# Kernel optimization log

Measured on AMD Instinct MI355X. Metric: run time of the kernel, lower is better.

The kernel has to match this reference:

```python
import math
import jax, jax.numpy as jnp
import numpy as np


def setup_inputs() -> dict:
    key = jax.random.key(0)
    T, C = 8192, 2048
    layer_depth, num_layers = 5, 10
    ks = jax.random.split(key, 8)

    x = jax.random.normal(ks[0], (T, C), jnp.float32)
    sx = jax.random.normal(ks[1], (C,), jnp.float32)
    aa = jnp.zeros((C,), jnp.float32)
    bb = jnp.zeros((C,), jnp.float32)
    pp = jnp.zeros((C,), jnp.float32)

    # parameter initial values per TimeMix.setup
    r01 = layer_depth / (num_layers - 1)
    r10 = 1.0 - layer_depth / num_layers
    zigzag = 0.5 * (jnp.arange(1, C + 1) % 3 - 1).astype(jnp.float32)
    time_first = jnp.full((C,), math.log(0.3), jnp.float32) + zigzag
    h = jnp.arange(C, dtype=jnp.float32)
    time_decay = (-5.0 + 8.0 * (h / (C - 1)) ** (0.7 + 1.3 * r01)).astype(jnp.float32)
    xr = jnp.arange(C, dtype=jnp.float32) / C
    time_mix_k = xr ** r10
    time_mix_v = time_mix_k + 0.3 * r01
    time_mix_r = xr ** (0.5 * r10)

    ln_scale = jnp.ones((C,), jnp.float32)
    ln_bias = jnp.zeros((C,), jnp.float32)

    s = 1.0 / np.sqrt(C)  # lecun-normal-ish scale for Dense kernels
    Wk = jax.random.normal(ks[2], (C, C), jnp.float32) * s
    Wv = jax.random.normal(ks[3], (C, C), jnp.float32) * s
    Wr = jax.random.normal(ks[4], (C, C), jnp.float32) * s
    Wo = jax.random.normal(ks[5], (C, C), jnp.float32) * s

    return dict(x=x, sx=sx, aa=aa, bb=bb, pp=pp,
                time_first=time_first, time_decay=time_decay,
                time_mix_k=time_mix_k, time_mix_v=time_mix_v, time_mix_r=time_mix_r,
                ln_scale=ln_scale, ln_bias=ln_bias,
                Wk=Wk, Wv=Wv, Wr=Wr, Wo=Wo)


def reference(x, sx, aa, bb, pp, time_first, time_decay,
              time_mix_k, time_mix_v, time_mix_r,
              ln_scale, ln_bias, Wk, Wv, Wr, Wo):
    # LayerNorm(eps=1e-5)
    mu = jnp.mean(x, axis=-1, keepdims=True)
    var = jnp.var(x, axis=-1, keepdims=True)
    xx = (x - mu) * jax.lax.rsqrt(var + 1e-5) * ln_scale + ln_bias  # [T, C]

    # token shift: previous timestep (sx state for t=0)
    sxs = jnp.concatenate((sx[None, :], xx[:-1, :]), axis=0)  # [T, C]
    kx = xx * time_mix_k + sxs * (1.0 - time_mix_k)
    vx = xx * time_mix_v + sxs * (1.0 - time_mix_v)
    rx = xx * time_mix_r + sxs * (1.0 - time_mix_r)

    r = jax.nn.sigmoid(rx @ Wr)  # [T, C]
    k = kx @ Wk                  # [T, C]
    v = vx @ Wv                  # [T, C]

    w = -jnp.exp(time_decay)     # [C]

    def step(state, kv):
        aa, bb, pp = state
        kk, vv = kv
        # output with numerically-stable log-sum-exp style bookkeeping
        ww = time_first + kk
        p = jnp.maximum(pp, ww)
        e1 = jnp.exp(pp - p)
        e2 = jnp.exp(ww - p)
        out = ((e1 * aa + e2 * vv) / (e1 * bb + e2)).astype(r.dtype)
        # state update
        ww2 = w + pp
        p2 = jnp.maximum(ww2, kk)
        e1b = jnp.exp(ww2 - p2)
        e2b = jnp.exp(kk - p2)
        aa = e1b * aa + e2b * vv
        bb = e1b * bb + e2b
        return (aa, bb, p2), out

    (aa, bb, pp), wkv = jax.lax.scan(step, (aa, bb, pp), (k, v))  # wkv: [T, C]

    out = x + (r * wkv) @ Wo
    return (out, xx[-1, :], aa, bb, pp)
```

## Files before the change

### kernel.cpp

```cpp
#include <hip/hip_runtime.h>
#include <stdint.h>

#define T_DIM 8192
#define C_DIM 2048
#define LCHUNK 128
#define NCHUNK (T_DIM / LCHUNK)

typedef unsigned short u16;
typedef __bf16 bf16x8_t __attribute__((ext_vector_type(8)));
typedef float f32x4_t __attribute__((ext_vector_type(4)));

__device__ __forceinline__ u16 f2bf(float f) {
    union { float f; uint32_t u; } x; x.f = f;
    uint32_t r = x.u + 0x7fffu + ((x.u >> 16) & 1u);
    return (u16)(r >> 16);
}
__device__ __forceinline__ float bf2f(u16 u) {
    union { uint32_t u; float f; } x; x.u = ((uint32_t)u) << 16;
    return x.f;
}
__device__ __forceinline__ void gload16(const void* g, void* l) {
    __builtin_amdgcn_global_load_lds((const __attribute__((address_space(1))) uint32_t*)g,
                                     (__attribute__((address_space(3))) uint32_t*)l, 16, 0, 0);
}
__device__ __forceinline__ f32x4_t mfma16(bf16x8_t a, bf16x8_t b, f32x4_t c) {
    return __builtin_amdgcn_mfma_f32_16x16x32_bf16(a, b, c, 0, 0, 0);
}

__global__ __launch_bounds__(256)
void transpose_cast(const float* __restrict__ W0, const float* __restrict__ W1,
                    const float* __restrict__ W2, const float* __restrict__ W3,
                    u16* __restrict__ Wt)
{
    __shared__ float tile[32][33];
    const int z = blockIdx.z;
    const float* W = (z == 0) ? W0 : (z == 1) ? W1 : (z == 2) ? W2 : W3;
    u16* Tm = Wt + (size_t)z * C_DIM * C_DIM;
    const int tx = threadIdx.x & 31, ty = threadIdx.x >> 5;
    const int bn = blockIdx.x * 32, bk = blockIdx.y * 32;
#pragma unroll
    for (int i = 0; i < 4; ++i)
        tile[ty + 8 * i][tx] = W[(size_t)(bk + ty + 8 * i) * C_DIM + bn + tx];
    __syncthreads();
#pragma unroll
    for (int i = 0; i < 4; ++i)
        Tm[(size_t)(bn + ty + 8 * i) * C_DIM + bk + tx] = f2bf(tile[tx][ty + 8 * i]);
}

union F8 { float4 v[2]; float f[8]; };

__global__ __launch_bounds__(256)
void ln_mix_kernel(const float* __restrict__ x, const float* __restrict__ sx,
                   const float* __restrict__ lns, const float* __restrict__ lnb,
                   const float* __restrict__ tmk, const float* __restrict__ tmv,
                   const float* __restrict__ tmr,
                   u16* __restrict__ kx, u16* __restrict__ vx, u16* __restrict__ rx,
                   float* __restrict__ xx_last)
{
    const int t = blockIdx.x;
    const int tid = threadIdx.x;
    const size_t rowoff = (size_t)t * C_DIM;

    F8 a, p;
    const float4* xt = (const float4*)(x + rowoff);
    a.v[0] = xt[2 * tid]; a.v[1] = xt[2 * tid + 1];
    const float4* xp = (t == 0) ? (const float4*)sx : (const float4*)(x + rowoff - C_DIM);
    p.v[0] = xp[2 * tid]; p.v[1] = xp[2 * tid + 1];

    float s1 = 0.f, s2 = 0.f, s3 = 0.f, s4 = 0.f;
#pragma unroll
    for (int i = 0; i < 8; ++i) {
        s1 += a.f[i]; s2 += a.f[i] * a.f[i];
        s3 += p.f[i]; s4 += p.f[i] * p.f[i];
    }
#pragma unroll
    for (int off = 32; off; off >>= 1) {
        s1 += __shfl_down(s1, off);
        s2 += __shfl_down(s2, off);
        s3 += __shfl_down(s3, off);
        s4 += __shfl_down(s4, off);
    }
    __shared__ float red[4][4];
    if ((tid & 63) == 0) {
        red[0][tid >> 6] = s1; red[1][tid >> 6] = s2;
        red[2][tid >> 6] = s3; red[3][tid >> 6] = s4;
    }
    __syncthreads();
    s1 = red[0][0] + red[0][1] + red[0][2] + red[0][3];
    s2 = red[1][0] + red[1][1] + red[1][2] + red[1][3];
    s3 = red[2][0] + red[2][1] + red[2][2] + red[2][3];
    s4 = red[3][0] + red[3][1] + red[3][2] + red[3][3];
    const float inv = 1.0f / (float)C_DIM;
    const float mu = s1 * inv;
    const float rstd = rsqrtf(s2 * inv - mu * mu + 1e-5f);
    const float mup = s3 * inv;
    const float rstdp = rsqrtf(s4 * inv - mup * mup + 1e-5f);

    F8 ls, lb, mk, mv, mr;
    { const float4* q = (const float4*)lns; ls.v[0] = q[2*tid]; ls.v[1] = q[2*tid+1]; }
    { const float4* q = (const float4*)lnb; lb.v[0] = q[2*tid]; lb.v[1] = q[2*tid+1]; }
    { const float4* q = (const float4*)tmk; mk.v[0] = q[2*tid]; mk.v[1] = q[2*tid+1]; }
    { const float4* q = (const float4*)tmv; mv.v[0] = q[2*tid]; mv.v[1] = q[2*tid+1]; }
    { const float4* q = (const float4*)tmr; mr.v[0] = q[2*tid]; mr.v[1] = q[2*tid+1]; }

    union { u16 u[8]; uint4 q; } ok, ov, orr;
#pragma unroll
    for (int i = 0; i < 8; ++i) {
        const float xxv  = (a.f[i] - mu) * rstd * ls.f[i] + lb.f[i];
        const float prev = (t == 0) ? p.f[i] : (p.f[i] - mup) * rstdp * ls.f[i] + lb.f[i];
        ok.u[i]  = f2bf(xxv * mk.f[i] + prev * (1.f - mk.f[i]));
        ov.u[i]  = f2bf(xxv * mv.f[i] + prev * (1.f - mv.f[i]));
        orr.u[i] = f2bf(xxv * mr.f[i] + prev * (1.f - mr.f[i]));
        if (t == T_DIM - 1) xx_last[tid * 8 + i] = xxv;
    }
    ((uint4*)(kx + rowoff))[tid] = ok.q;
    ((uint4*)(vx + rowoff))[tid] = ov.q;
    ((uint4*)(rx + rowoff))[tid] = orr.q;
}

__global__ __launch_bounds__(256, 2)
void gemm_tile(const u16* __restrict__ A, const u16* __restrict__ Bt,
               void* __restrict__ Cout, const float* __restrict__ resid,
               const int mode, const int M, const int N, const int K)
{
    __shared__ u16 lds[2 * 12288];
    const int tid = threadIdx.x;
    const int wave = tid >> 6, lane = tid & 63;
    const int nbm = M >> 8;
    const int m0 = (int)(blockIdx.x % nbm) << 8;
    const int n0 = (int)(blockIdx.x / nbm) << 7;
    const int wm = wave >> 1, wn = wave & 1;
    const int fr = lane & 15, fo = lane >> 4;
    const int sw = (fo ^ ((fr >> 1) & 3)) * 8;

    f32x4_t acc[8][4] = {};

    const int lrow = lane >> 2;
    const int scol = ((lane & 3) ^ ((lane >> 3) & 3)) * 8;
    const u16* gA = A  + (size_t)(m0 + wave * 16 + lrow) * K + scol;
    const u16* gB = Bt + (size_t)(n0 + wave * 16 + lrow) * K + scol;
    const int dstw = wave * 512;

    auto stage = [&](int t) {
        const int b = (t & 1) * 12288;
        const u16* ga = gA + (size_t)t * 32;
        const u16* gb = gB + (size_t)t * 32;
        gload16(ga,                   lds + b + dstw);
        gload16(ga + (size_t)64 * K,  lds + b + 2048 + dstw);
        gload16(ga + (size_t)128 * K, lds + b + 4096 + dstw);
        gload16(ga + (size_t)192 * K, lds + b + 6144 + dstw);
        gload16(gb,                   lds + b + 8192 + dstw);
        gload16(gb + (size_t)64 * K,  lds + b + 10240 + dstw);
    };

    const int NT = K >> 5;
    stage(0);
    asm volatile("s_waitcnt vmcnt(0)" ::: "memory");
    asm volatile("s_barrier" ::: "memory");

    for (int t = 0; t < NT; ++t) {
        if (t + 1 < NT) stage(t + 1);
        const u16* lA = lds + (t & 1) * 12288 + (wm * 128 + fr) * 32;
        const u16* lB = lds + (t & 1) * 12288 + 8192 + (wn * 64 + fr) * 32;
        bf16x8_t a[8], b[4];
#pragma unroll
        for (int mi = 0; mi < 8; ++mi) a[mi] = *(const bf16x8_t*)(lA + mi * 512 + sw);
#pragma unroll
        for (int ni = 0; ni < 4; ++ni) b[ni] = *(const bf16x8_t*)(lB + ni * 512 + sw);
        __builtin_amdgcn_s_setprio(1);
#pragma unroll
        for (int mi = 0; mi < 8; ++mi)
#pragma unroll
            for (int ni = 0; ni < 4; ++ni)
                acc[mi][ni] = mfma16(a[mi], b[ni], acc[mi][ni]);
        __builtin_amdgcn_s_setprio(0);
        asm volatile("s_waitcnt vmcnt(0)" ::: "memory");
        asm volatile("s_barrier" ::: "memory");
    }

    const int r4 = fo * 4;
#pragma unroll
    for (int mi = 0; mi < 8; ++mi) {
#pragma unroll
        for (int ni = 0; ni < 4; ++ni) {
            const int col = n0 + wn * 64 + ni * 16 + fr;
#pragma unroll
            for (int i = 0; i < 4; ++i) {
                const int row = m0 + wm * 128 + mi * 16 + r4 + i;
                float v = acc[mi][ni][i];
                if (resid) v += resid[(size_t)row * N + col];
                if (mode == 0)      ((float*)Cout)[(size_t)row * N + col] = v;
                else if (mode == 1) ((u16*)Cout)[(size_t)row * N + col] = f2bf(v);
                else {
                    const float s = 1.f / (1.f + __expf(-v));
                    ((u16*)Cout)[(size_t)row * N + col] = f2bf(s);
                }
            }
        }
    }
}

__global__ __launch_bounds__(256)
void scan_partial(const float* __restrict__ k, const u16* __restrict__ v,
                  const float* __restrict__ time_decay,
                  float* __restrict__ pA, float* __restrict__ pB, float* __restrict__ pP)
{
    const int c = blockIdx.y * 256 + threadIdx.x;
    const int j = blockIdx.x;
    const float w = -__expf(time_decay[c]);
    float aa = 0.f, bb = 0.f, pp = -1e30f;
    const float* kp = k + (size_t)j * LCHUNK * C_DIM + c;
    const u16*  vp = v + (size_t)j * LCHUNK * C_DIM + c;
#pragma unroll 4
    for (int i = 0; i < LCHUNK; ++i) {
        const float kk = *kp;
        const float vv = bf2f(*vp);
        kp += C_DIM; vp += C_DIM;
        const float ww = w + pp;
        const float p2 = fmaxf(ww, kk);
        const float e1 = __expf(ww - p2);
        const float e2 = __expf(kk - p2);
        aa = e1 * aa + e2 * vv;
        bb = e1 * bb + e2;
        pp = p2;
    }
    const int o = j * C_DIM + c;
    pA[o] = aa; pB[o] = bb; pP[o] = pp;
}

__global__ __launch_bounds__(256)
void scan_combine(const float* __restrict__ pA, const float* __restrict__ pB,
                  const float* __restrict__ pP,
                  const float* __restrict__ aa_in, const float* __restrict__ bb_in,
                  const float* __restrict__ pp_in,
                  const float* __restrict__ time_decay,
                  float* __restrict__ sA, float* __restrict__ sB, float* __restrict__ sP)
{
    const int c = blockIdx.x * 256 + threadIdx.x;
    const float wL = -__expf(time_decay[c]) * (float)LCHUNK;
    float a = aa_in[c], b = bb_in[c], p = pp_in[c];
    for (int j = 0; j < NCHUNK; ++j) {
        const int o = j * C_DIM + c;
        sA[o] = a; sB[o] = b; sP[o] = p;
        const float A = pA[o], B = pB[o], P = pP[o];
        const float pd = p + wL;
        const float q = fmaxf(pd, P);
        const float e1 = __expf(pd - q), e2 = __expf(P - q);
        a = e1 * a + e2 * A;
        b = e1 * b + e2 * B;
        p = q;
    }
}

__global__ __launch_bounds__(256)
void scan_out(const float* __restrict__ k, const u16* __restrict__ v,
              const u16* __restrict__ r,
              const float* __restrict__ time_decay, const float* __restrict__ time_first,
              const float* __restrict__ sA, const float* __restrict__ sB,
              const float* __restrict__ sP,
              u16* __restrict__ arwkv,
              float* __restrict__ aa_out, float* __restrict__ bb_out, float* __restrict__ pp_out)
{
    const int c = blockIdx.y * 256 + threadIdx.x;
    const int j = blockIdx.x;
    const float w = -__expf(time_decay[c]);
    const float u = time_first[c];
    const int so = j * C_DIM + c;
    float aa = sA[so], bb = sB[so], pp = sP[so];
    const size_t base = (size_t)j * LCHUNK * C_DIM + c;
    const float* kp = k + base;
    const u16*  vp = v + base;
    const u16*  rp = r + base;
    u16* op = arwkv + base;
#pragma unroll 4
    for (int i = 0; i < LCHUNK; ++i) {
        const float kk = *kp;
        const float vv = bf2f(*vp);
        const float sr = bf2f(*rp);
        kp += C_DIM; vp += C_DIM; rp += C_DIM;
        const float ww = u + kk;
        const float p = fmaxf(pp, ww);
        const float e1 = __expf(pp - p);
        const float e2 = __expf(ww - p);
        const float out = (e1 * aa + e2 * vv) / (e1 * bb + e2);
        *op = f2bf(sr * out);
        op += C_DIM;
        const float ww2 = w + pp;
        const float p2 = fmaxf(ww2, kk);
        const float f1 = __expf(ww2 - p2);
        const float f2 = __expf(kk - p2);
        aa = f1 * aa + f2 * vv;
        bb = f1 * bb + f2;
        pp = p2;
    }
    if (j == NCHUNK - 1) { aa_out[c] = aa; bb_out[c] = bb; pp_out[c] = pp; }
}

extern "C" void kernel_launch(void* const* d_in, const int* in_sizes, int n_in,
                              void* d_out, int out_size, void* d_ws, size_t ws_size,
                              hipStream_t stream)
{
    (void)in_sizes; (void)n_in; (void)out_size; (void)ws_size;
    const float* x          = (const float*)d_in[0];
    const float* sx         = (const float*)d_in[1];
    const float* aa_in      = (const float*)d_in[2];
    const float* bb_in      = (const float*)d_in[3];
    const float* pp_in      = (const float*)d_in[4];
    const float* time_first = (const float*)d_in[5];
    const float* time_decay = (const float*)d_in[6];
    const float* tmk        = (const float*)d_in[7];
    const float* tmv        = (const float*)d_in[8];
    const float* tmr        = (const float*)d_in[9];
    const float* lns        = (const float*)d_in[10];
    const float* lnb        = (const float*)d_in[11];
    const float* Wk         = (const float*)d_in[12];
    const float* Wv         = (const float*)d_in[13];
    const float* Wr         = (const float*)d_in[14];
    const float* Wo         = (const float*)d_in[15];

    float* out     = (float*)d_out;
    float* xx_last = out + (size_t)T_DIM * C_DIM;
    float* aa_out  = xx_last + C_DIM;
    float* bb_out  = aa_out + C_DIM;
    float* pp_out  = bb_out + C_DIM;

    const size_t TC = (size_t)T_DIM * C_DIM;
    const size_t C2 = (size_t)C_DIM * C_DIM;
    u16* kx    = (u16*)d_ws;
    u16* vx    = kx + TC;
    u16* rx    = vx + TC;
    u16* Wt    = rx + TC;
    float* kbuf = (float*)(Wt + 4 * C2);
    u16* vbuf   = (u16*)(kbuf + TC);
    float* pA   = (float*)(vbuf + TC);
    float* pB   = pA + (size_t)NCHUNK * C_DIM;
    float* pP   = pB + (size_t)NCHUNK * C_DIM;
    float* sA   = pP + (size_t)NCHUNK * C_DIM;
    float* sB   = sA + (size_t)NCHUNK * C_DIM;
    float* sP   = sB + (size_t)NCHUNK * C_DIM;
    u16* rbuf   = kx;
    u16* arwkv  = rx;

    transpose_cast<<<dim3(C_DIM / 32, C_DIM / 32, 4), 256, 0, stream>>>(Wk, Wv, Wr, Wo, Wt);
    ln_mix_kernel<<<T_DIM, 256, 0, stream>>>(x, sx, lns, lnb, tmk, tmv, tmr, kx, vx, rx, xx_last);

    const int NWG = (T_DIM / 256) * (C_DIM / 128);
    gemm_tile<<<NWG, 256, 0, stream>>>(kx, Wt + 0 * C2, kbuf, nullptr, 0, T_DIM, C_DIM, C_DIM);
    gemm_tile<<<NWG, 256, 0, stream>>>(vx, Wt + 1 * C2, vbuf, nullptr, 1, T_DIM, C_DIM, C_DIM);
    gemm_tile<<<NWG, 256, 0, stream>>>(rx, Wt + 2 * C2, rbuf, nullptr, 2, T_DIM, C_DIM, C_DIM);

    scan_partial<<<dim3(NCHUNK, C_DIM / 256), 256, 0, stream>>>(kbuf, vbuf, time_decay, pA, pB, pP);
    scan_combine<<<C_DIM / 256, 256, 0, stream>>>(pA, pB, pP, aa_in, bb_in, pp_in, time_decay, sA, sB, sP);
    scan_out<<<dim3(NCHUNK, C_DIM / 256), 256, 0, stream>>>(kbuf, vbuf, rbuf, time_decay, time_first,
                                                            sA, sB, sP, arwkv, aa_out, bb_out, pp_out);

    gemm_tile<<<NWG, 256, 0, stream>>>(arwkv, Wt + 3 * C2, out, x, 0, T_DIM, C_DIM, C_DIM);
}
```

Measured before the change: 487.8 us.

## Use barrier-free per-wave GEMM tiles, batch k/v/r GEMMs, store k as bf16

The GEMM is restructured so each wave stages its own 64x64 A/B slices into a private double-buffered LDS region. That removes block-wide barriers, at the cost of duplicated global loads across waves and no LDS swizzle. The block tile shrinks from 256x128 to 128x128. The k, v and r projections are merged into one launch via a grid y-dimension, and k is now written as bf16 instead of fp32. The bf16 k cuts scan memory traffic but lowers the precision of k feeding the exp-based recurrence.

New measurement: 640.7 us. 1.31x slower.

```diff
diff --git a/kernel.cpp b/kernel.cpp
--- a/kernel.cpp
+++ b/kernel.cpp
@@ -118,75 +118,70 @@
     ((uint4*)(rx + rowoff))[tid] = orr.q;
 }
 
-__global__ __launch_bounds__(256, 2)
-void gemm_tile(const u16* __restrict__ A, const u16* __restrict__ Bt,
-               void* __restrict__ Cout, const float* __restrict__ resid,
-               const int mode, const int M, const int N, const int K)
-{
-    __shared__ u16 lds[2 * 12288];
+__device__ __forceinline__ void gemm_core(
+    const u16* __restrict__ A, const u16* __restrict__ Bt,
+    void* __restrict__ Cout, const float* __restrict__ resid,
+    const int mode, const int N, const int K,
+    const int m0, const int n0, u16* lds)
+{
     const int tid = threadIdx.x;
     const int wave = tid >> 6, lane = tid & 63;
-    const int nbm = M >> 8;
-    const int m0 = (int)(blockIdx.x % nbm) << 8;
-    const int n0 = (int)(blockIdx.x / nbm) << 7;
     const int wm = wave >> 1, wn = wave & 1;
     const int fr = lane & 15, fo = lane >> 4;
-    const int sw = (fo ^ ((fr >> 1) & 3)) * 8;
-
-    f32x4_t acc[8][4] = {};
-
+
+    f32x4_t acc[4][4] = {};
+
+    u16* wl = lds + wave * 8192;
     const int lrow = lane >> 2;
-    const int scol = ((lane & 3) ^ ((lane >> 3) & 3)) * 8;
-    const u16* gA = A  + (size_t)(m0 + wave * 16 + lrow) * K + scol;
-    const u16* gB = Bt + (size_t)(n0 + wave * 16 + lrow) * K + scol;
-    const int dstw = wave * 512;
+    const int lcol8 = (lane & 3) * 8;
+    const u16* gA = A  + (size_t)(m0 + wm * 64 + lrow) * K + lcol8;
+    const u16* gB = Bt + (size_t)(n0 + wn * 64 + lrow) * K + lcol8;
+    const size_t rk16 = (size_t)16 * K;
 
     auto stage = [&](int t) {
-        const int b = (t & 1) * 12288;
-        const u16* ga = gA + (size_t)t * 32;
-        const u16* gb = gB + (size_t)t * 32;
-        gload16(ga,                   lds + b + dstw);
-        gload16(ga + (size_t)64 * K,  lds + b + 2048 + dstw);
-        gload16(ga + (size_t)128 * K, lds + b + 4096 + dstw);
-        gload16(ga + (size_t)192 * K, lds + b + 6144 + dstw);
-        gload16(gb,                   lds + b + 8192 + dstw);
-        gload16(gb + (size_t)64 * K,  lds + b + 10240 + dstw);
+        u16* d = wl + (t & 1) * 4096 + lane * 8;
+        const u16* a = gA + (size_t)t * 32;
+        const u16* b = gB + (size_t)t * 32;
+        gload16(a,            d);
+        gload16(a + rk16,     d + 512);
+        gload16(a + 2 * rk16, d + 1024);
+        gload16(a + 3 * rk16, d + 1536);
+        gload16(b,            d + 2048);
+        gload16(b + rk16,     d + 2560);
+        gload16(b + 2 * rk16, d + 3072);
+        gload16(b + 3 * rk16, d + 3584);
     };
 
     const int NT = K >> 5;
     stage(0);
-    asm volatile("s_waitcnt vmcnt(0)" ::: "memory");
-    asm volatile("s_barrier" ::: "memory");
-
     for (int t = 0; t < NT; ++t) {
-        if (t + 1 < NT) stage(t + 1);
-        const u16* lA = lds + (t & 1) * 12288 + (wm * 128 + fr) * 32;
-        const u16* lB = lds + (t & 1) * 12288 + 8192 + (wn * 64 + fr) * 32;
-        bf16x8_t a[8], b[4];
-#pragma unroll
-        for (int mi = 0; mi < 8; ++mi) a[mi] = *(const bf16x8_t*)(lA + mi * 512 + sw);
-#pragma unroll
-        for (int ni = 0; ni < 4; ++ni) b[ni] = *(const bf16x8_t*)(lB + ni * 512 + sw);
+        if (t + 1 < NT) { stage(t + 1); asm volatile("s_waitcnt vmcnt(8)" ::: "memory"); }
+        else            { asm volatile("s_waitcnt vmcnt(0)" ::: "memory"); }
+        const u16* lb = wl + (t & 1) * 4096;
+        bf16x8_t a[4], b[4];
+#pragma unroll
+        for (int i = 0; i < 4; ++i) {
+            a[i] = *(const bf16x8_t*)(lb + i * 512 + fr * 32 + fo * 8);
+            b[i] = *(const bf16x8_t*)(lb + 2048 + i * 512 + fr * 32 + fo * 8);
+        }
         __builtin_amdgcn_s_setprio(1);
 #pragma unroll
-        for (int mi = 0; mi < 8; ++mi)
+        for (int mi = 0; mi < 4; ++mi)
 #pragma unroll
             for (int ni = 0; ni < 4; ++ni)
                 acc[mi][ni] = mfma16(a[mi], b[ni], acc[mi][ni]);
         __builtin_amdgcn_s_setprio(0);
-        asm volatile("s_waitcnt vmcnt(0)" ::: "memory");
-        asm volatile("s_barrier" ::: "memory");
     }
 
     const int r4 = fo * 4;
 #pragma unroll
-    for (int mi = 0; mi < 8; ++mi) {
+    for (int mi = 0; mi < 4; ++mi) {
 #pragma unroll
         for (int ni = 0; ni < 4; ++ni) {
             const int col = n0 + wn * 64 + ni * 16 + fr;
 #pragma unroll
             for (int i = 0; i < 4; ++i) {
-                const int row = m0 + wm * 128 + mi * 16 + r4 + i;
+                const int row = m0 + wm * 64 + mi * 16 + r4 + i;
                 float v = acc[mi][ni][i];
                 if (resid) v += resid[(size_t)row * N + col];
                 if (mode == 0)      ((float*)Cout)[(size_t)row * N + col] = v;
@@ -200,8 +195,33 @@
     }
 }
 
-__global__ __launch_bounds__(256)
-void scan_partial(const float* __restrict__ k, const u16* __restrict__ v,
+__global__ __launch_bounds__(256, 2)
+void gemm_kvr(const u16* __restrict__ kx, const u16* __restrict__ vx, const u16* __restrict__ rxp,
+              const u16* __restrict__ Wt,
+              u16* __restrict__ kbuf, u16* __restrict__ vbuf, u16* __restrict__ rbuf)
+{
+    __shared__ u16 lds[32768];
+    const int which = blockIdx.y;
+    const int m0 = (int)(blockIdx.x & 63) << 7;
+    const int n0 = (int)(blockIdx.x >> 6) << 7;
+    const u16* A = (which == 0) ? kx : (which == 1) ? vx : rxp;
+    const u16* B = Wt + (size_t)which * C_DIM * C_DIM;
+    u16* C = (which == 0) ? kbuf : (which == 1) ? vbuf : rbuf;
+    gemm_core(A, B, C, nullptr, (which == 2) ? 2 : 1, C_DIM, C_DIM, m0, n0, lds);
+}
+
+__global__ __launch_bounds__(256, 2)
+void gemm_o(const u16* __restrict__ Aw, const u16* __restrict__ Wt3,
+            float* __restrict__ out, const float* __restrict__ x)
+{
+    __shared__ u16 lds[32768];
+    const int m0 = (int)(blockIdx.x & 63) << 7;
+    const int n0 = (int)(blockIdx.x >> 6) << 7;
+    gemm_core(Aw, Wt3, out, x, 0, C_DIM, C_DIM, m0, n0, lds);
+}
+
+__global__ __launch_bounds__(256)
+void scan_partial(const u16* __restrict__ k, const u16* __restrict__ v,
                   const float* __restrict__ time_decay,
                   float* __restrict__ pA, float* __restrict__ pB, float* __restrict__ pP)
 {
@@ -209,11 +229,11 @@
     const int j = blockIdx.x;
     const float w = -__expf(time_decay[c]);
     float aa = 0.f, bb = 0.f, pp = -1e30f;
-    const float* kp = k + (size_t)j * LCHUNK * C_DIM + c;
-    const u16*  vp = v + (size_t)j * LCHUNK * C_DIM + c;
+    const u16* kp = k + (size_t)j * LCHUNK * C_DIM + c;
+    const u16* vp = v + (size_t)j * LCHUNK * C_DIM + c;
 #pragma unroll 4
     for (int i = 0; i < LCHUNK; ++i) {
-        const float kk = *kp;
+        const float kk = bf2f(*kp);
         const float vv = bf2f(*vp);
         kp += C_DIM; vp += C_DIM;
         const float ww = w + pp;
@@ -253,7 +273,7 @@
 }
 
 __global__ __launch_bounds__(256)
-void scan_out(const float* __restrict__ k, const u16* __restrict__ v,
+void scan_out(const u16* __restrict__ k, const u16* __restrict__ v,
               const u16* __restrict__ r,
               const float* __restrict__ time_decay, const float* __restrict__ time_first,
               const float* __restrict__ sA, const float* __restrict__ sB,
@@ -268,13 +288,13 @@
     const int so = j * C_DIM + c;
     float aa = sA[so], bb = sB[so], pp = sP[so];
     const size_t base = (size_t)j * LCHUNK * C_DIM + c;
-    const float* kp = k + base;
-    const u16*  vp = v + base;
-    const u16*  rp = r + base;
+    const u16* kp = k + base;
+    const u16* vp = v + base;
+    const u16* rp = r + base;
     u16* op = arwkv + base;
 #pragma unroll 4
     for (int i = 0; i < LCHUNK; ++i) {
-        const float kk = *kp;
+        const float kk = bf2f(*kp);
         const float vv = bf2f(*vp);
         const float sr = bf2f(*rp);
         kp += C_DIM; vp += C_DIM; rp += C_DIM;
@@ -330,29 +350,27 @@
     u16* vx    = kx + TC;
     u16* rx    = vx + TC;
     u16* Wt    = rx + TC;
-    float* kbuf = (float*)(Wt + 4 * C2);
-    u16* vbuf   = (u16*)(kbuf + TC);
-    float* pA   = (float*)(vbuf + TC);
-    float* pB   = pA + (size_t)NCHUNK * C_DIM;
-    float* pP   = pB + (size_t)NCHUNK * C_DIM;
-    float* sA   = pP + (size_t)NCHUNK * C_DIM;
-    float* sB   = sA + (size_t)NCHUNK * C_DIM;
-    float* sP   = sB + (size_t)NCHUNK * C_DIM;
-    u16* rbuf   = kx;
-    u16* arwkv  = rx;
+    u16* kbuf  = Wt + 4 * C2;
+    u16* vbuf  = kbuf + TC;
+    u16* rbuf  = vbuf + TC;
+    float* pA  = (float*)(rbuf + TC);
+    float* pB  = pA + (size_t)NCHUNK * C_DIM;
+    float* pP  = pB + (size_t)NCHUNK * C_DIM;
+    float* sA  = pP + (size_t)NCHUNK * C_DIM;
+    float* sB  = sA + (size_t)NCHUNK * C_DIM;
+    float* sP  = sB + (size_t)NCHUNK * C_DIM;
+    u16* arwkv = rx;
 
     transpose_cast<<<dim3(C_DIM / 32, C_DIM / 32, 4), 256, 0, stream>>>(Wk, Wv, Wr, Wo, Wt);
     ln_mix_kernel<<<T_DIM, 256, 0, stream>>>(x, sx, lns, lnb, tmk, tmv, tmr, kx, vx, rx, xx_last);
 
-    const int NWG = (T_DIM / 256) * (C_DIM / 128);
-    gemm_tile<<<NWG, 256, 0, stream>>>(kx, Wt + 0 * C2, kbuf, nullptr, 0, T_DIM, C_DIM, C_DIM);
-    gemm_tile<<<NWG, 256, 0, stream>>>(vx, Wt + 1 * C2, vbuf, nullptr, 1, T_DIM, C_DIM, C_DIM);
-    gemm_tile<<<NWG, 256, 0, stream>>>(rx, Wt + 2 * C2, rbuf, nullptr, 2, T_DIM, C_DIM, C_DIM);
+    const int NB = (T_DIM / 128) * (C_DIM / 128);
+    gemm_kvr<<<dim3(NB, 3), 256, 0, stream>>>(kx, vx, rx, Wt, kbuf, vbuf, rbuf);
 
     scan_partial<<<dim3(NCHUNK, C_DIM / 256), 256, 0, stream>>>(kbuf, vbuf, time_decay, pA, pB, pP);
     scan_combine<<<C_DIM / 256, 256, 0, stream>>>(pA, pB, pP, aa_in, bb_in, pp_in, time_decay, sA, sB, sP);
     scan_out<<<dim3(NCHUNK, C_DIM / 256), 256, 0, stream>>>(kbuf, vbuf, rbuf, time_decay, time_first,
                                                             sA, sB, sP, arwkv, aa_out, bb_out, pp_out);
 
-    gemm_tile<<<NWG, 256, 0, stream>>>(arwkv, Wt + 3 * C2, out, x, 0, T_DIM, C_DIM, C_DIM);
-}
+    gemm_o<<<NB, 256, 0, stream>>>(arwkv, Wt + 3 * C2, out, x);
+}
```
